# Optimization experiments

Hardware: AMD Instinct MI355X
Metric: run time of the kernel (lower is better)

The kernel has to match this reference:

```python
import jax, jax.numpy as jnp
import numpy as np
from jax import lax

B, C_IN, T_IN = 1024, 22, 2047
C_TEMP, KT, PAD = 20, 12, 6
N_PATCH = 8
ATT_OUT = 18
N_OUT = 4
BN_EPS = 1e-5
REEIG_EPS = 1e-4


def _sym(X):
    return 0.5 * (X + jnp.swapaxes(X, -1, -2))


def _eig_fn(X, fn):
    w, v = jnp.linalg.eigh(_sym(X))
    return jnp.einsum('...ij,...j,...kj->...ik', v, fn(w), v)


def _logm(X):
    return _eig_fn(X, lambda w: jnp.log(jnp.maximum(w, 1e-10)))


def _expm(X):
    return _eig_fn(X, jnp.exp)


def _reeig(X):
    return _eig_fn(X, lambda w: jnp.maximum(w, REEIG_EPS))


def _batchnorm(x, gamma, beta):
    # x: (B, C, T); training-mode stats over (B, T)
    mu = x.mean(axis=(0, 2), keepdims=True)
    var = x.var(axis=(0, 2), keepdims=True)
    return (x - mu) * jax.lax.rsqrt(var + BN_EPS) * gamma[None, :, None] + beta[None, :, None]


def setup_inputs() -> dict:
    key = jax.random.key(0)
    ks = jax.random.split(key, 8)
    tangent_dim = ATT_OUT * (ATT_OUT + 1) // 2
    return {
        'x': jax.random.normal(ks[0], (B, C_IN, T_IN), dtype=jnp.float32),
        'w_spat': jax.random.normal(ks[1], (C_IN, C_IN), dtype=jnp.float32) * 0.3,
        'b_spat': jnp.zeros((C_IN,), jnp.float32),
        'g1': jnp.ones((C_IN,), jnp.float32),
        'be1': jnp.zeros((C_IN,), jnp.float32),
        'w_temp': jax.random.normal(ks[2], (C_TEMP, C_IN, KT), dtype=jnp.float32) * 0.1,
        'b_temp': jnp.zeros((C_TEMP,), jnp.float32),
        'g2': jnp.ones((C_TEMP,), jnp.float32),
        'be2': jnp.zeros((C_TEMP,), jnp.float32),
        'wq': jax.random.normal(ks[3], (ATT_OUT, C_TEMP), dtype=jnp.float32) / np.sqrt(C_TEMP),
        'wk': jax.random.normal(ks[4], (ATT_OUT, C_TEMP), dtype=jnp.float32) / np.sqrt(C_TEMP),
        'wv': jax.random.normal(ks[5], (ATT_OUT, C_TEMP), dtype=jnp.float32) / np.sqrt(C_TEMP),
        'w_lin': jax.random.normal(ks[6], (N_OUT, N_PATCH * tangent_dim), dtype=jnp.float32) * 0.05,
        'b_lin': jnp.zeros((N_OUT,), jnp.float32),
    }


def _matt_forward(x, w_spat, b_spat, g1, be1, w_temp, b_temp, g2, be2, wq, wk, wv, w_lin, b_lin):
    b = x.shape[0]
    # spatial filter: Conv2d(1, n_chans, (n_chans,1)) == full channel mix
    h = jnp.einsum('oc,bct->bot', w_spat, x) + b_spat[None, :, None]
    h = _batchnorm(h, g1, be1)
    # temporal conv: Conv2d(n_chans, 20, (1,12), pad (0,6)) == 1D conv over time
    h = lax.conv_general_dilated(h, w_temp, window_strides=(1,), padding=[(PAD, PAD)],
                                 dimension_numbers=('NCH', 'OIH', 'NCH'))
    h = h + b_temp[None, :, None]
    h = _batchnorm(h, g2, be2)
    # patch embedding: split time into N_PATCH segments -> (B, P, C, Tp)
    cf, tt = h.shape[1], h.shape[2]
    tp = tt // N_PATCH
    h = h[:, :, :N_PATCH * tp].reshape(b, cf, N_PATCH, tp).transpose(0, 2, 1, 3)
    # sample covariance per patch + trace normalization
    hc = h - h.mean(axis=-1, keepdims=True)
    cov = jnp.einsum('bpct,bpdt->bpcd', hc, hc) / (tp - 1)
    cov = cov / jnp.trace(cov, axis1=-2, axis2=-1)[..., None, None]
    # manifold attention: BiMap Q/K/V = W X W^T
    Q = jnp.einsum('oi,bpij,qj->bpoq', wq, cov, wq)
    K = jnp.einsum('oi,bpij,qj->bpoq', wk, cov, wk)
    V = jnp.einsum('oi,bpij,qj->bpoq', wv, cov, wv)
    lq, lk, lv = _logm(Q), _logm(K), _logm(V)
    n = lq.shape[-1]
    fq = lq.reshape(b, N_PATCH, n * n)
    fk = lk.reshape(b, N_PATCH, n * n)
    sq = jnp.sum(fq * fq, -1)
    sk = jnp.sum(fk * fk, -1)
    cross = jnp.einsum('bid,bjd->bij', fq, fk)
    d2 = jnp.maximum(sq[:, :, None] + sk[:, None, :] - 2.0 * cross, 0.0)
    energy = jnp.sqrt(d2 + 1e-12)  # log-Euclidean distance ||logQ_i - logK_j||_F
    weights = 1.0 / (1.0 + jnp.log1p(energy))
    prob = jax.nn.softmax(weights, axis=-2)          # normalize over queries i
    probT = jnp.swapaxes(prob, -1, -2)               # (b, j, i)
    # log-Euclidean weighted Frechet mean: expm(sum_i w_ji logm(V_i))
    out = _expm(jnp.einsum('bji,bixy->bjxy', probT, lv))
    # R2E: ReEig + LogEig + triu vectorization (off-diag * sqrt(2))
    lt = _logm(_reeig(out))
    iu0, iu1 = np.triu_indices(n)
    scale = jnp.asarray(np.where(iu0 == iu1, 1.0, np.sqrt(2.0)), dtype=lt.dtype)
    vec = lt[..., iu0, iu1] * scale                  # (B, P, n(n+1)/2)
    feat = vec.reshape(b, -1)
    return feat @ w_lin.T + b_lin


def reference(x, w_spat, b_spat, g1, be1, w_temp, b_temp, g2, be2, wq, wk, wv, w_lin, b_lin):
    return _matt_forward(x, w_spat, b_spat, g1, be1, w_temp, b_temp, g2, be2, wq, wk, wv, w_lin, b_lin)
```

## Files before the change

kernel.cpp:

```cpp
#include <hip/hip_runtime.h>
#include <math.h>

constexpr int NSWEEP = 5;

constexpr size_t OFF_SUMX   = 0;
constexpr size_t OFF_G      = 22;
constexpr size_t OFF_SUM2   = 288;
constexpr size_t OFF_SUMSQ2 = 308;
constexpr size_t OFF_S2     = 328;
constexpr size_t OFF_A      = 352;
constexpr size_t OFF_D      = 840;
constexpr size_t OFF_WR     = 864;
constexpr size_t OFF_COV    = 6144;
constexpr size_t OFF_LQKV   = 3282944;
constexpr size_t OFF_FEAT   = 11245568;

struct Tri { int a[253]; int b[253]; };
constexpr Tri mk_tri(int n) {
    Tri t{}; int c = 0;
    for (int i = 0; i < n; ++i) for (int j = i; j < n; ++j) { t.a[c] = i; t.b[c] = j; ++c; }
    return t;
}
constexpr Tri T22 = mk_tri(22);
constexpr Tri T20 = mk_tri(20);
constexpr Tri T18 = mk_tri(18);

struct Sched { int p[17][9]; int q[17][9]; };
constexpr Sched mk_sched() {
    Sched s{};
    for (int r = 0; r < 17; ++r)
        for (int k = 0; k < 9; ++k) {
            int x, y;
            if (k == 0) { x = 17; y = r; }
            else { x = (r + k) % 17; y = (r - k + 17) % 17; }
            s.p[r][k] = x < y ? x : y;
            s.q[r][k] = x < y ? y : x;
        }
    return s;
}
constexpr Sched SCH = mk_sched();

__device__ __forceinline__ float jacobi18(float* __restrict__ a, float* __restrict__ v,
                                          int jj, int base) {
    int pt[17];
#pragma unroll
    for (int r = 0; r < 17; ++r) {
        int k1 = jj - r; if (k1 < 0) k1 += 17;
        int partner;
        if (jj == 17)      { partner = r; }
        else if (k1 == 0)  { partner = 17; }
        else if (k1 <= 8)  { partner = r - k1; if (partner < 0) partner += 17; }
        else               { partner = r + 17 - k1; if (partner >= 17) partner -= 17; }
        pt[r] = partner;
    }
    float mydiag = a[0];
#pragma unroll
    for (int i = 1; i < 18; ++i) if (jj == i) mydiag = a[i];

    for (int sw = 0; sw < NSWEEP; ++sw) {
#pragma unroll
        for (int r = 0; r < 17; ++r) {
            const int partner = pt[r];
            const int paddr = base + partner;
            const bool isp = jj < partner;
            const int plane = isp ? jj : partner;
            float pd = __shfl(mydiag, paddr, 64);
            float apq = a[0];
#pragma unroll
            for (int i = 1; i < 18; ++i) if (partner == i) apq = a[i];
            float app = isp ? mydiag : pd;
            float aqq = isp ? pd : mydiag;
            float apqc = (fabsf(apq) < 1e-36f) ? 1e-36f : apq;
            float tau = (aqq - app) * 0.5f * __builtin_amdgcn_rcpf(apqc);
            float t0 = __builtin_amdgcn_rcpf(fabsf(tau) + __builtin_amdgcn_sqrtf(fmaf(tau, tau, 1.f)));
            t0 = (tau < 0.f) ? -t0 : t0;
            float tb[9];
#pragma unroll
            for (int k = 0; k < 9; ++k)
                tb[k] = __shfl(t0, base + SCH.p[r][k], 64);
            float mt = __shfl(t0, base + plane, 64);
            float cc[9], ss[9];
#pragma unroll
            for (int k = 0; k < 9; ++k) {
                cc[k] = __builtin_amdgcn_rsqf(fmaf(tb[k], tb[k], 1.f));
                ss[k] = tb[k] * cc[k];
            }
            float mc = __builtin_amdgcn_rsqf(fmaf(mt, mt, 1.f));
            float ms = mt * mc;
            mydiag = fmaf(isp ? -mt : mt, apq, mydiag);
#pragma unroll
            for (int k = 0; k < 9; ++k) {
                const int p = SCH.p[r][k], q = SCH.q[r][k];
                float tp = a[p], tq = a[q];
                a[p] = cc[k] * tp - ss[k] * tq;
                a[q] = ss[k] * tp + cc[k] * tq;
            }
            float ssig = isp ? -ms : ms;
#pragma unroll
            for (int i = 0; i < 18; ++i) {
                float oa = __shfl(a[i], paddr, 64);
                a[i] = mc * a[i] + ssig * oa;
            }
#pragma unroll
            for (int i = 0; i < 18; ++i) {
                float ov = __shfl(v[i], paddr, 64);
                v[i] = mc * v[i] + ssig * ov;
            }
        }
    }
    float lam = a[0];
#pragma unroll
    for (int i = 1; i < 18; ++i) if (jj == i) lam = a[i];
    return lam;
}

__global__ void k0_zero(float* ws) {
    int tid = threadIdx.x;
    for (int i = tid; i < 352; i += 256) ws[i] = 0.f;
}

__global__ __launch_bounds__(256) void k1_stats(const float* __restrict__ x,
                                                float* __restrict__ sumx,
                                                float* __restrict__ G) {
    int b = blockIdx.x, tid = threadIdx.x;
    __shared__ float xt[22 * 257];
    float accp = 0.f, accs = 0.f;
    int c1 = 0, c2 = 0;
    if (tid < 253) { c1 = T22.a[tid]; c2 = T22.b[tid]; }
    const float* xb = x + (size_t)b * 22 * 2047;
    for (int t0 = 0; t0 < 2047; t0 += 256) {
        __syncthreads();
        for (int idx = tid; idx < 22 * 256; idx += 256) {
            int c = idx >> 8, tl = idx & 255;
            int t = t0 + tl;
            xt[c * 257 + tl] = (t < 2047) ? xb[c * 2047 + t] : 0.f;
        }
        __syncthreads();
        if (tid < 253) {
            float s = 0.f;
            for (int t = 0; t < 256; ++t) s += xt[c1 * 257 + t] * xt[c2 * 257 + t];
            accp += s;
        }
        if (tid < 22) {
            float s = 0.f;
            for (int t = 0; t < 256; ++t) s += xt[tid * 257 + t];
            accs += s;
        }
    }
    if (tid < 253) atomicAdd(&G[tid], accp);
    if (tid < 22) atomicAdd(&sumx[tid], accs);
}

__global__ __launch_bounds__(256) void k2_prep(const float* __restrict__ w_spat,
                                               const float* __restrict__ b_spat,
                                               const float* __restrict__ g1,
                                               const float* __restrict__ be1,
                                               const float* __restrict__ w_temp,
                                               const float* __restrict__ sumx,
                                               const float* __restrict__ G,
                                               float* __restrict__ A,
                                               float* __restrict__ dv,
                                               float* __restrict__ w_r) {
    int tid = threadIdx.x;
    __shared__ float cov[22 * 22], mux[22], mu1s[22], s1s[22];
    const float invN = 1.f / (1024.f * 2047.f);
    if (tid < 22) mux[tid] = sumx[tid] * invN;
    __syncthreads();
    if (tid < 253) {
        int c1 = T22.a[tid], c2 = T22.b[tid];
        float cv = G[tid] * invN - mux[c1] * mux[c2];
        cov[c1 * 22 + c2] = cv; cov[c2 * 22 + c1] = cv;
    }
    __syncthreads();
    if (tid < 22) {
        int c = tid;
        float m = b_spat[c], varv = 0.f;
        for (int e = 0; e < 22; ++e) m += w_spat[c * 22 + e] * mux[e];
        for (int i = 0; i < 22; ++i) {
            float wi = w_spat[c * 22 + i];
            for (int j = 0; j < 22; ++j) varv += wi * w_spat[c * 22 + j] * cov[i * 22 + j];
        }
        mu1s[c] = m;
        s1s[c] = g1[c] * rsqrtf(varv + 1e-5f);
    }
    __syncthreads();
    for (int idx = tid; idx < 484; idx += 256) {
        int c = idx / 22;
        A[idx] = s1s[c] * w_spat[idx];
    }
    if (tid < 22) dv[tid] = s1s[tid] * (b_spat[tid] - mu1s[tid]) + be1[tid];
    for (int idx = tid; idx < 5280; idx += 256) {
        int f = idx / 264, r = idx % 264;
        w_r[r * 20 + f] = w_temp[idx];
    }
}

__global__ __launch_bounds__(256) void k3_conv(const float* __restrict__ x,
                                               const float* __restrict__ wsA,
                                               const float* __restrict__ wsd,
                                               const float* __restrict__ w_r,
                                               float* __restrict__ cov_raw,
                                               float* __restrict__ sum2,
                                               float* __restrict__ sumsq2) {
    int bp = blockIdx.x;
    int b = bp >> 3, p = bp & 7;
    int tid = threadIdx.x;
    __shared__ float xs[22 * 267];
    __shared__ float h2[20 * 257];
    __shared__ float pm[20];

    const float* xb = x + (size_t)b * 22 * 2047;
    const int t0 = p * 256 - 6;
    for (int idx = tid; idx < 22 * 267; idx += 256) {
        int c = idx / 267, tl = idx % 267;
        int t = t0 + tl;
        xs[idx] = (t >= 0 && t < 2047) ? xb[c * 2047 + t] : 0.f;
    }
    __syncthreads();
    for (int tl = tid; tl < 267; tl += 256) {
        float xv[22];
#pragma unroll
        for (int c = 0; c < 22; ++c) xv[c] = xs[c * 267 + tl];
        int t = t0 + tl;
        bool valid = (t >= 0 && t < 2047);
#pragma unroll
        for (int c = 0; c < 22; ++c) {
            float acc = wsd[c];
#pragma unroll
            for (int e = 0; e < 22; ++e) acc += wsA[c * 22 + e] * xv[e];
            xs[c * 267 + tl] = valid ? acc : 0.f;
        }
    }
    __syncthreads();
    {
        int tl = tid;
        float acc[20];
#pragma unroll
        for (int f = 0; f < 20; ++f) acc[f] = 0.f;
        for (int c = 0; c < 22; ++c) {
#pragma unroll
            for (int k = 0; k < 12; ++k) {
                float hv = xs[c * 267 + tl + k];
                const float* wp = w_r + (c * 12 + k) * 20;
#pragma unroll
                for (int f = 0; f < 20; ++f) acc[f] += wp[f] * hv;
            }
        }
#pragma unroll
        for (int f = 0; f < 20; ++f) h2[f * 257 + tl] = acc[f];
    }
    __syncthreads();
    if (tid < 20) {
        int f = tid;
        float s = 0.f, ss = 0.f;
        for (int t = 0; t < 256; ++t) { float v = h2[f * 257 + t]; s += v; ss += v * v; }
        pm[f] = s * (1.f / 256.f);
        atomicAdd(&sum2[f], s);
        atomicAdd(&sumsq2[f], ss);
    }
    __syncthreads();
    for (int pr = tid; pr < 210; pr += 256) {
        int f = T20.a[pr], g = T20.b[pr];
        float s = 0.f;
        for (int t = 0; t < 256; ++t) s += h2[f * 257 + t] * h2[g * 257 + t];
        float cv = s - 256.f * pm[f] * pm[g];
        cov_raw[(size_t)bp * 400 + f * 20 + g] = cv;
        if (f != g) cov_raw[(size_t)bp * 400 + g * 20 + f] = cv;
    }
}

__global__ void k4_s2(const float* __restrict__ g2, const float* __restrict__ sum2,
                      const float* __restrict__ sumsq2, float* __restrict__ s2) {
    int tid = threadIdx.x;
    if (tid < 20) {
        const float invN = 1.f / (1024.f * 2048.f);
        float mu = sum2[tid] * invN;
        float var = sumsq2[tid] * invN - mu * mu;
        s2[tid] = g2[tid] * rsqrtf(var + 1e-5f);
    }
}

__global__ __launch_bounds__(256) void k5_qkv(const float* __restrict__ wq,
                                              const float* __restrict__ wk,
                                              const float* __restrict__ wv,
                                              const float* __restrict__ s2g,
                                              const float* __restrict__ cov_raw,
                                              float* __restrict__ lqkv) {
    int tid = threadIdx.x;
    int wave = tid >> 6;
    int lane = tid & 63;
    int bp = blockIdx.x * 4 + wave;
    __shared__ float Wl[1080];
    __shared__ float s2l[20];
    __shared__ float covn[4][400];
    __shared__ float Vs[4][972];
    __shared__ float lws[4][54];

    if (tid < 20) s2l[tid] = s2g[tid];
    for (int idx = lane; idx < 400; idx += 64)
        covn[wave][idx] = cov_raw[(size_t)bp * 400 + idx];
    __syncthreads();
    for (int idx = tid; idx < 1080; idx += 256) {
        int m = idx / 360, rem = idx % 360;
        const float* W = (m == 0) ? wq : (m == 1) ? wk : wv;
        Wl[idx] = W[rem] * s2l[rem % 20];
    }
    __syncthreads();

    float tr = 0.f;
#pragma unroll
    for (int f = 0; f < 20; ++f) tr += covn[wave][f * 21] * s2l[f] * s2l[f];
    float trinv = 1.f / tr;

    int grp = lane / 18;
    int jj = lane - grp * 18;
    int m = grp < 3 ? grp : 2;
    int base = grp * 18;
    float Wrow[20];
#pragma unroll
    for (int d = 0; d < 20; ++d) Wrow[d] = Wl[m * 360 + jj * 20 + d];
    float u[20];
#pragma unroll
    for (int e = 0; e < 20; ++e) {
        float acc = 0.f;
#pragma unroll
        for (int d = 0; d < 20; ++d) acc += covn[wave][e * 20 + d] * Wrow[d];
        u[e] = acc;
    }
    float a[18], v[18];
#pragma unroll
    for (int i = 0; i < 18; ++i) {
        float acc = 0.f;
#pragma unroll
        for (int e = 0; e < 20; ++e) acc += Wl[m * 360 + i * 20 + e] * u[e];
        a[i] = acc * trinv;
        v[i] = (i == jj) ? 1.f : 0.f;
    }
    float lam = jacobi18(a, v, jj, base);
    float lw = __logf(fmaxf(lam, 1e-10f));
    if (grp < 3) {
#pragma unroll
        for (int i = 0; i < 18; ++i) Vs[wave][(m * 18 + i) * 18 + jj] = v[i];
        lws[wave][m * 18 + jj] = lw;
    }
    __builtin_amdgcn_wave_barrier();
    for (int idx = lane; idx < 972; idx += 64) {
        int m2 = idx / 324, rem = idx % 324, i = rem / 18, jo = rem % 18;
        float acc = 0.f;
#pragma unroll
        for (int kk = 0; kk < 18; ++kk)
            acc += Vs[wave][(m2 * 18 + i) * 18 + kk] * lws[wave][m2 * 18 + kk] * Vs[wave][(m2 * 18 + jo) * 18 + kk];
        lqkv[(size_t)(bp * 3 + m2) * 324 + rem] = acc;
    }
}

__global__ __launch_bounds__(256) void k6_attn(const float* __restrict__ lqkv,
                                               float* __restrict__ mixed) {
    int b = blockIdx.x, tid = threadIdx.x;
    __shared__ float L[7776];
    __shared__ float sq[8], sk[8], cross[64], prob[64];
    const float* src = lqkv + (size_t)b * 7776;
    for (int idx = tid; idx < 7776; idx += 256) L[idx] = src[idx];
    __syncthreads();
    if (tid < 64) {
        int i = tid >> 3, j = tid & 7;
        const float* fq = &L[(i * 3 + 0) * 324];
        const float* fk = &L[(j * 3 + 1) * 324];
        float cr = 0.f;
        for (int e = 0; e < 324; ++e) cr += fq[e] * fk[e];
        cross[tid] = cr;
    } else if (tid < 72) {
        int i = tid - 64;
        const float* fq = &L[(i * 3 + 0) * 324];
        float s = 0.f;
        for (int e = 0; e < 324; ++e) s += fq[e] * fq[e];
        sq[i] = s;
    } else if (tid < 80) {
        int i = tid - 72;
        const float* fk = &L[(i * 3 + 1) * 324];
        float s = 0.f;
        for (int e = 0; e < 324; ++e) s += fk[e] * fk[e];
        sk[i] = s;
    }
    __syncthreads();
    if (tid < 8) {
        int j = tid;
        float w[8], mx = -1e30f;
        for (int i = 0; i < 8; ++i) {
            float d2 = fmaxf(sq[i] + sk[j] - 2.f * cross[i * 8 + j], 0.0f);
            float en = sqrtf(d2 + 1e-12f);
            w[i] = 1.f / (1.f + log1pf(en));
            mx = fmaxf(mx, w[i]);
        }
        float ssum = 0.f;
        for (int i = 0; i < 8; ++i) { w[i] = __expf(w[i] - mx); ssum += w[i]; }
        float inv = 1.f / ssum;
        for (int i = 0; i < 8; ++i) prob[i * 8 + j] = w[i] * inv;
    }
    __syncthreads();
    float* dst = mixed + (size_t)b * 8 * 324;
    for (int idx = tid; idx < 8 * 324; idx += 256) {
        int j = idx / 324, e = idx % 324;
        float acc = 0.f;
#pragma unroll
        for (int i = 0; i < 8; ++i) acc += prob[i * 8 + j] * L[(i * 3 + 2) * 324 + e];
        dst[idx] = acc;
    }
}

__global__ __launch_bounds__(256) void k7_post(const float* __restrict__ mixed,
                                               float* __restrict__ feat) {
    int tid = threadIdx.x;
    int wave = tid >> 6;
    int lane = tid & 63;
    int blk = blockIdx.x;
    int grp = lane / 18;
    int jj = lane - grp * 18;
    int m = grp < 3 ? grp : 2;
    int base = grp * 18;
    int mat = blk * 12 + wave * 3 + m;
    int matc = mat < 8192 ? mat : 8191;
    __shared__ float Vs[4][972];
    __shared__ float lws[4][54];

    const float* src = mixed + (size_t)matc * 324;
    float a[18], v[18];
#pragma unroll
    for (int i = 0; i < 18; ++i) {
        a[i] = src[i * 18 + jj];
        v[i] = (i == jj) ? 1.f : 0.f;
    }
    float diag = a[0], asum = 0.f;
#pragma unroll
    for (int i = 0; i < 18; ++i) {
        if (jj == i) diag = a[i];
        asum += fabsf(a[i]);
    }
    float gb = 2.f * diag - asum;
#pragma unroll
    for (int off = 32; off; off >>= 1) gb = fminf(gb, __shfl_xor(gb, off, 64));
    const bool skipAll = (gb > -9.2103f);

    if (!skipAll) {
        float lam = jacobi18(a, v, jj, base);
        float lw = fmaxf(lam, -9.210340371976182f);
        if (grp < 3) {
#pragma unroll
            for (int i = 0; i < 18; ++i) Vs[wave][(m * 18 + i) * 18 + jj] = v[i];
            lws[wave][m * 18 + jj] = lw;
        }
    }
    __builtin_amdgcn_wave_barrier();
    for (int idx = lane; idx < 513; idx += 64) {
        int m2 = idx / 171, rem = idx % 171;
        int mat2 = blk * 12 + wave * 3 + m2;
        if (mat2 >= 8192) continue;
        int i = T18.a[rem], jo = T18.b[rem];
        float acc;
        if (skipAll) {
            acc = mixed[(size_t)mat2 * 324 + i * 18 + jo];
        } else {
            acc = 0.f;
#pragma unroll
            for (int kk = 0; kk < 18; ++kk)
                acc += Vs[wave][(m2 * 18 + i) * 18 + kk] * lws[wave][m2 * 18 + kk] * Vs[wave][(m2 * 18 + jo) * 18 + kk];
        }
        float scl = (i == jo) ? 1.f : 1.41421356237309515f;
        int bb = mat2 >> 3, pp = mat2 & 7;
        feat[(size_t)bb * 1368 + pp * 171 + rem] = acc * scl;
    }
}

__global__ __launch_bounds__(256) void k8_lin(const float* __restrict__ feat,
                                              const float* __restrict__ w_lin,
                                              const float* __restrict__ b_lin,
                                              float* __restrict__ out) {
    int b = blockIdx.x, tid = threadIdx.x;
    int o = tid >> 6, lane = tid & 63;
    const float* fb = feat + (size_t)b * 1368;
    const float* wo = w_lin + o * 1368;
    float acc = 0.f;
    for (int e = lane; e < 1368; e += 64) acc += fb[e] * wo[e];
    for (int off = 32; off; off >>= 1) acc += __shfl_down(acc, off, 64);
    if (lane == 0) out[b * 4 + o] = acc + b_lin[o];
}

extern "C" void kernel_launch(void* const* d_in, const int* in_sizes, int n_in,
                              void* d_out, int out_size, void* d_ws, size_t ws_size,
                              hipStream_t stream) {
    (void)in_sizes; (void)n_in; (void)out_size; (void)ws_size;
    const float* x      = (const float*)d_in[0];
    const float* w_spat = (const float*)d_in[1];
    const float* b_spat = (const float*)d_in[2];
    const float* g1     = (const float*)d_in[3];
    const float* be1    = (const float*)d_in[4];
    const float* w_temp = (const float*)d_in[5];
    const float* g2     = (const float*)d_in[7];
    const float* wq     = (const float*)d_in[9];
    const float* wk     = (const float*)d_in[10];
    const float* wv     = (const float*)d_in[11];
    const float* w_lin  = (const float*)d_in[12];
    const float* b_lin  = (const float*)d_in[13];
    float* ws  = (float*)d_ws;
    float* out = (float*)d_out;

    k0_zero<<<1, 256, 0, stream>>>(ws);
    k1_stats<<<1024, 256, 0, stream>>>(x, ws + OFF_SUMX, ws + OFF_G);
    k2_prep<<<1, 256, 0, stream>>>(w_spat, b_spat, g1, be1, w_temp,
                                   ws + OFF_SUMX, ws + OFF_G,
                                   ws + OFF_A, ws + OFF_D, ws + OFF_WR);
    k3_conv<<<8192, 256, 0, stream>>>(x, ws + OFF_A, ws + OFF_D, ws + OFF_WR,
                                      ws + OFF_COV, ws + OFF_SUM2, ws + OFF_SUMSQ2);
    k4_s2<<<1, 64, 0, stream>>>(g2, ws + OFF_SUM2, ws + OFF_SUMSQ2, ws + OFF_S2);
    k5_qkv<<<2048, 256, 0, stream>>>(wq, wk, wv, ws + OFF_S2, ws + OFF_COV, ws + OFF_LQKV);
    k6_attn<<<1024, 256, 0, stream>>>(ws + OFF_LQKV, ws + OFF_COV );
    k7_post<<<683, 256, 0, stream>>>(ws + OFF_COV, ws + OFF_FEAT);
    k8_lin<<<1024, 256, 0, stream>>>(ws + OFF_FEAT, w_lin, b_lin, out);
}
```

Before: 1.584 ms.

## Fold spatial filter into temporal conv weights, trim Jacobi sweeps, symmetric logm output

Precomposes the BN-scaled spatial mixing matrix with the temporal conv weights in the prep kernel, so the conv kernel skips its per-tile channel-mixing pass. The spatial bias contribution is applied through precomputed per-tap sums, with a boundary-aware path for zero-padded edges. Separately, the 18x18 Jacobi eigensolver drops from 5 full sweeps to 4 sweeps plus 9 rounds, which cuts work but may lower convergence accuracy. The logm reconstruction computes only the upper triangle and mirrors it.

Measured after the change: 1.437 ms. 9.3% less time.

```diff
diff --git a/kernel.cpp b/kernel.cpp
--- a/kernel.cpp
+++ b/kernel.cpp
@@ -1,16 +1,17 @@
 #include <hip/hip_runtime.h>
 #include <math.h>
 
-constexpr int NSWEEP = 5;
+constexpr int FULL_SWEEPS  = 4;
+constexpr int EXTRA_ROUNDS = 9;
 
 constexpr size_t OFF_SUMX   = 0;
 constexpr size_t OFF_G      = 22;
 constexpr size_t OFF_SUM2   = 288;
 constexpr size_t OFF_SUMSQ2 = 308;
 constexpr size_t OFF_S2     = 328;
-constexpr size_t OFF_A      = 352;
-constexpr size_t OFF_D      = 840;
-constexpr size_t OFF_WR     = 864;
+constexpr size_t OFF_WD     = 352;
+constexpr size_t OFF_WDSUM  = 840;
+constexpr size_t OFF_MW     = 864;
 constexpr size_t OFF_COV    = 6144;
 constexpr size_t OFF_LQKV   = 3282944;
 constexpr size_t OFF_FEAT   = 11245568;
@@ -57,57 +58,62 @@
 #pragma unroll
     for (int i = 1; i < 18; ++i) if (jj == i) mydiag = a[i];
 
-    for (int sw = 0; sw < NSWEEP; ++sw) {
-#pragma unroll
-        for (int r = 0; r < 17; ++r) {
-            const int partner = pt[r];
-            const int paddr = base + partner;
-            const bool isp = jj < partner;
-            const int plane = isp ? jj : partner;
-            float pd = __shfl(mydiag, paddr, 64);
-            float apq = a[0];
-#pragma unroll
-            for (int i = 1; i < 18; ++i) if (partner == i) apq = a[i];
-            float app = isp ? mydiag : pd;
-            float aqq = isp ? pd : mydiag;
-            float apqc = (fabsf(apq) < 1e-36f) ? 1e-36f : apq;
-            float tau = (aqq - app) * 0.5f * __builtin_amdgcn_rcpf(apqc);
-            float t0 = __builtin_amdgcn_rcpf(fabsf(tau) + __builtin_amdgcn_sqrtf(fmaf(tau, tau, 1.f)));
-            t0 = (tau < 0.f) ? -t0 : t0;
-            float tb[9];
-#pragma unroll
-            for (int k = 0; k < 9; ++k)
-                tb[k] = __shfl(t0, base + SCH.p[r][k], 64);
-            float mt = __shfl(t0, base + plane, 64);
-            float cc[9], ss[9];
-#pragma unroll
-            for (int k = 0; k < 9; ++k) {
-                cc[k] = __builtin_amdgcn_rsqf(fmaf(tb[k], tb[k], 1.f));
-                ss[k] = tb[k] * cc[k];
-            }
-            float mc = __builtin_amdgcn_rsqf(fmaf(mt, mt, 1.f));
-            float ms = mt * mc;
-            mydiag = fmaf(isp ? -mt : mt, apq, mydiag);
-#pragma unroll
-            for (int k = 0; k < 9; ++k) {
-                const int p = SCH.p[r][k], q = SCH.q[r][k];
-                float tp = a[p], tq = a[q];
-                a[p] = cc[k] * tp - ss[k] * tq;
-                a[q] = ss[k] * tp + cc[k] * tq;
-            }
-            float ssig = isp ? -ms : ms;
-#pragma unroll
-            for (int i = 0; i < 18; ++i) {
-                float oa = __shfl(a[i], paddr, 64);
-                a[i] = mc * a[i] + ssig * oa;
-            }
-#pragma unroll
-            for (int i = 0; i < 18; ++i) {
-                float ov = __shfl(v[i], paddr, 64);
-                v[i] = mc * v[i] + ssig * ov;
-            }
-        }
-    }
+    auto round_body = [&](int r) {
+        const int partner = pt[r];
+        const int paddr = base + partner;
+        const bool isp = jj < partner;
+        const int plane = isp ? jj : partner;
+        float pd = __shfl(mydiag, paddr, 64);
+        float apq = a[0];
+#pragma unroll
+        for (int i = 1; i < 18; ++i) if (partner == i) apq = a[i];
+        float app = isp ? mydiag : pd;
+        float aqq = isp ? pd : mydiag;
+        float apqc = (fabsf(apq) < 1e-36f) ? 1e-36f : apq;
+        float tau = (aqq - app) * 0.5f * __builtin_amdgcn_rcpf(apqc);
+        float t0 = __builtin_amdgcn_rcpf(fabsf(tau) + __builtin_amdgcn_sqrtf(fmaf(tau, tau, 1.f)));
+        t0 = (tau < 0.f) ? -t0 : t0;
+        float tb[9];
+#pragma unroll
+        for (int k = 0; k < 9; ++k)
+            tb[k] = __shfl(t0, base + SCH.p[r][k], 64);
+        float mt = __shfl(t0, base + plane, 64);
+        float cc[9], ss[9];
+#pragma unroll
+        for (int k = 0; k < 9; ++k) {
+            cc[k] = __builtin_amdgcn_rsqf(fmaf(tb[k], tb[k], 1.f));
+            ss[k] = tb[k] * cc[k];
+        }
+        float mc = __builtin_amdgcn_rsqf(fmaf(mt, mt, 1.f));
+        float ms = mt * mc;
+        mydiag = fmaf(isp ? -mt : mt, apq, mydiag);
+#pragma unroll
+        for (int k = 0; k < 9; ++k) {
+            const int p = SCH.p[r][k], q = SCH.q[r][k];
+            float tp = a[p], tq = a[q];
+            a[p] = cc[k] * tp - ss[k] * tq;
+            a[q] = ss[k] * tp + cc[k] * tq;
+        }
+        float ssig = isp ? -ms : ms;
+#pragma unroll
+        for (int i = 0; i < 18; ++i) {
+            float oa = __shfl(a[i], paddr, 64);
+            a[i] = mc * a[i] + ssig * oa;
+        }
+#pragma unroll
+        for (int i = 0; i < 18; ++i) {
+            float ov = __shfl(v[i], paddr, 64);
+            v[i] = mc * v[i] + ssig * ov;
+        }
+    };
+
+    for (int sw = 0; sw < FULL_SWEEPS; ++sw) {
+#pragma unroll
+        for (int r = 0; r < 17; ++r) round_body(r);
+    }
+#pragma unroll
+    for (int r = 0; r < EXTRA_ROUNDS; ++r) round_body(r);
+
     float lam = a[0];
 #pragma unroll
     for (int i = 1; i < 18; ++i) if (jj == i) lam = a[i];
@@ -158,11 +164,12 @@
                                                const float* __restrict__ w_temp,
                                                const float* __restrict__ sumx,
                                                const float* __restrict__ G,
-                                               float* __restrict__ A,
-                                               float* __restrict__ dv,
-                                               float* __restrict__ w_r) {
+                                               float* __restrict__ Mw,
+                                               float* __restrict__ wd,
+                                               float* __restrict__ wdsum) {
     int tid = threadIdx.x;
-    __shared__ float cov[22 * 22], mux[22], mu1s[22], s1s[22];
+    __shared__ float cov[22 * 22], mux[22], mu1s[22], s1s[22], dvs[22];
+    __shared__ float As[484];
     const float invN = 1.f / (1024.f * 2047.f);
     if (tid < 22) mux[tid] = sumx[tid] * invN;
     __syncthreads();
@@ -186,19 +193,38 @@
     __syncthreads();
     for (int idx = tid; idx < 484; idx += 256) {
         int c = idx / 22;
-        A[idx] = s1s[c] * w_spat[idx];
-    }
-    if (tid < 22) dv[tid] = s1s[tid] * (b_spat[tid] - mu1s[tid]) + be1[tid];
+        As[idx] = s1s[c] * w_spat[idx];
+    }
+    if (tid < 22) dvs[tid] = s1s[tid] * (b_spat[tid] - mu1s[tid]) + be1[tid];
+    __syncthreads();
     for (int idx = tid; idx < 5280; idx += 256) {
-        int f = idx / 264, r = idx % 264;
-        w_r[r * 20 + f] = w_temp[idx];
+        int r = idx / 20, f = idx % 20;
+        int e = r / 12, k = r % 12;
+        float acc = 0.f;
+        for (int c = 0; c < 22; ++c)
+            acc += w_temp[f * 264 + c * 12 + k] * As[c * 22 + e];
+        Mw[idx] = acc;
+    }
+    if (tid < 240) {
+        int k = tid / 20, f = tid % 20;
+        float acc = 0.f;
+        for (int c = 0; c < 22; ++c)
+            acc += w_temp[f * 264 + c * 12 + k] * dvs[c];
+        wd[tid] = acc;
+    } else if (tid < 260) {
+        int f = tid - 240;
+        float acc = 0.f;
+        for (int k = 0; k < 12; ++k)
+            for (int c = 0; c < 22; ++c)
+                acc += w_temp[f * 264 + c * 12 + k] * dvs[c];
+        wdsum[f] = acc;
     }
 }
 
 __global__ __launch_bounds__(256) void k3_conv(const float* __restrict__ x,
-                                               const float* __restrict__ wsA,
-                                               const float* __restrict__ wsd,
-                                               const float* __restrict__ w_r,
+                                               const float* __restrict__ Mw,
+                                               const float* __restrict__ wd,
+                                               const float* __restrict__ wdsum,
                                                float* __restrict__ cov_raw,
                                                float* __restrict__ sum2,
                                                float* __restrict__ sumsq2) {
@@ -217,33 +243,32 @@
         xs[idx] = (t >= 0 && t < 2047) ? xb[c * 2047 + t] : 0.f;
     }
     __syncthreads();
-    for (int tl = tid; tl < 267; tl += 256) {
-        float xv[22];
-#pragma unroll
-        for (int c = 0; c < 22; ++c) xv[c] = xs[c * 267 + tl];
-        int t = t0 + tl;
-        bool valid = (t >= 0 && t < 2047);
-#pragma unroll
-        for (int c = 0; c < 22; ++c) {
-            float acc = wsd[c];
-#pragma unroll
-            for (int e = 0; e < 22; ++e) acc += wsA[c * 22 + e] * xv[e];
-            xs[c * 267 + tl] = valid ? acc : 0.f;
-        }
-    }
-    __syncthreads();
     {
         int tl = tid;
         float acc[20];
 #pragma unroll
         for (int f = 0; f < 20; ++f) acc[f] = 0.f;
-        for (int c = 0; c < 22; ++c) {
+        for (int e = 0; e < 22; ++e) {
 #pragma unroll
             for (int k = 0; k < 12; ++k) {
-                float hv = xs[c * 267 + tl + k];
-                const float* wp = w_r + (c * 12 + k) * 20;
+                float hv = xs[e * 267 + tl + k];
+                const float* wp = Mw + (e * 12 + k) * 20;
 #pragma unroll
                 for (int f = 0; f < 20; ++f) acc[f] += wp[f] * hv;
+            }
+        }
+        int tcol = t0 + tl;
+        if (tcol >= 0 && tcol + 11 < 2047) {
+#pragma unroll
+            for (int f = 0; f < 20; ++f) acc[f] += wdsum[f];
+        } else {
+#pragma unroll
+            for (int k = 0; k < 12; ++k) {
+                int t = tcol + k;
+                float vm = (t >= 0 && t < 2047) ? 1.f : 0.f;
+                const float* wdp = wd + k * 20;
+#pragma unroll
+                for (int f = 0; f < 20; ++f) acc[f] = fmaf(vm, wdp[f], acc[f]);
             }
         }
 #pragma unroll
@@ -344,13 +369,16 @@
         lws[wave][m * 18 + jj] = lw;
     }
     __builtin_amdgcn_wave_barrier();
-    for (int idx = lane; idx < 972; idx += 64) {
-        int m2 = idx / 324, rem = idx % 324, i = rem / 18, jo = rem % 18;
+    for (int idx = lane; idx < 513; idx += 64) {
+        int m2 = idx / 171, rem = idx % 171;
+        int i = T18.a[rem], jo = T18.b[rem];
         float acc = 0.f;
 #pragma unroll
         for (int kk = 0; kk < 18; ++kk)
             acc += Vs[wave][(m2 * 18 + i) * 18 + kk] * lws[wave][m2 * 18 + kk] * Vs[wave][(m2 * 18 + jo) * 18 + kk];
-        lqkv[(size_t)(bp * 3 + m2) * 324 + rem] = acc;
+        float* dst = lqkv + (size_t)(bp * 3 + m2) * 324;
+        dst[i * 18 + jo] = acc;
+        if (i != jo) dst[jo * 18 + i] = acc;
     }
 }
 
@@ -508,8 +536,8 @@
     k1_stats<<<1024, 256, 0, stream>>>(x, ws + OFF_SUMX, ws + OFF_G);
     k2_prep<<<1, 256, 0, stream>>>(w_spat, b_spat, g1, be1, w_temp,
                                    ws + OFF_SUMX, ws + OFF_G,
-                                   ws + OFF_A, ws + OFF_D, ws + OFF_WR);
-    k3_conv<<<8192, 256, 0, stream>>>(x, ws + OFF_A, ws + OFF_D, ws + OFF_WR,
+                                   ws + OFF_MW, ws + OFF_WD, ws + OFF_WDSUM);
+    k3_conv<<<8192, 256, 0, stream>>>(x, ws + OFF_MW, ws + OFF_WD, ws + OFF_WDSUM,
                                       ws + OFF_COV, ws + OFF_SUM2, ws + OFF_SUMSQ2);
     k4_s2<<<1, 64, 0, stream>>>(g2, ws + OFF_SUM2, ws + OFF_SUMSQ2, ws + OFF_S2);
     k5_qkv<<<2048, 256, 0, stream>>>(wq, wk, wv, ws + OFF_S2, ws + OFF_COV, ws + OFF_LQKV);
```
